# Optimization experiments

Hardware: AMD Instinct MI355X
Metric: run time of the kernel (lower is better)

## Reference

```python
import jax, jax.numpy as jnp
import numpy as np

IN_F = 4096
OUT_F = 4096
NNZ = 1638400
TOKENS = 8192


def setup_inputs() -> dict:
    key = jax.random.key(0)
    k1, k2, k3, k4, k5 = jax.random.split(key, 5)
    x = jax.random.normal(k1, (TOKENS, IN_F), dtype=jnp.float32)
    weight_pruned = jax.random.normal(k2, (NNZ,), dtype=jnp.float32)
    bias = jax.random.normal(k3, (OUT_F,), dtype=jnp.float32)
    row_idx = jax.random.randint(k4, (NNZ,), 0, OUT_F, dtype=jnp.int32)
    col_idx = jax.random.randint(k5, (NNZ,), 0, IN_F, dtype=jnp.int32)
    return {"x": x, "weight_pruned": weight_pruned, "bias": bias,
            "row_idx": row_idx, "col_idx": col_idx}


def reference(x, weight_pruned, bias, row_idx, col_idx):
    # matching torch advanced-index assignment), then dense linear.
    W = jnp.zeros((OUT_F, IN_F), dtype=weight_pruned.dtype)
    W = W.at[row_idx, col_idx].set(weight_pruned)
    return x @ W.T + bias
```

## Files before the change

### kernel.cpp

```cpp
#include <hip/hip_runtime.h>
#include <hip/hip_bf16.h>
#include <cstdint>

#define TOKENS 8192
#define IN_F 4096
#define OUT_F 4096

typedef __bf16 bf16x8 __attribute__((ext_vector_type(8)));
typedef float f32x4 __attribute__((ext_vector_type(4)));

__global__ void scatter_max_kernel(const int* __restrict__ row,
                                   const int* __restrict__ col,
                                   int* __restrict__ M, int nnz) {
    int i = blockIdx.x * blockDim.x + threadIdx.x;
    if (i < nnz) {
        atomicMax(&M[(size_t)row[i] * IN_F + col[i]], i);
    }
}

__global__ void extract_convert_kernel(const int* __restrict__ M,
                                       const float* __restrict__ w,
                                       __bf16* __restrict__ Wb,
                                       const float* __restrict__ x,
                                       __bf16* __restrict__ xb,
                                       int eb) {
    if ((int)blockIdx.x < eb) {
        size_t base = ((size_t)blockIdx.x * 256 + threadIdx.x) * 8;
        int4 m0 = *(const int4*)(M + base);
        int4 m1 = *(const int4*)(M + base + 4);
        int idx[8] = {m0.x, m0.y, m0.z, m0.w, m1.x, m1.y, m1.z, m1.w};
        bf16x8 o;
#pragma unroll
        for (int j = 0; j < 8; ++j) {
            o[j] = (idx[j] >= 0) ? (__bf16)w[idx[j]] : (__bf16)0.0f;
        }
        *(bf16x8*)(Wb + base) = o;
    } else {
        size_t base = ((size_t)(blockIdx.x - eb) * 256 + threadIdx.x) * 8;
        float4 v0 = *(const float4*)(x + base);
        float4 v1 = *(const float4*)(x + base + 4);
        bf16x8 o;
        o[0] = (__bf16)v0.x; o[1] = (__bf16)v0.y;
        o[2] = (__bf16)v0.z; o[3] = (__bf16)v0.w;
        o[4] = (__bf16)v1.x; o[5] = (__bf16)v1.y;
        o[6] = (__bf16)v1.z; o[7] = (__bf16)v1.w;
        *(bf16x8*)(xb + base) = o;
    }
}

__global__ __launch_bounds__(256) void gemm_bt_kernel(
    const __bf16* __restrict__ A,
    const __bf16* __restrict__ B,
    const float* __restrict__ bias,
    float* __restrict__ C) {
    __shared__ __bf16 As[128 * 32];
    __shared__ __bf16 Bs[128 * 32];

    const int tid  = threadIdx.x;
    const int lane = tid & 63;
    const int wid  = tid >> 6;
    const int m0 = blockIdx.y * 128;
    const int n0 = blockIdx.x * 128;
    const int wm = (wid >> 1) * 64;
    const int wn = (wid & 1) * 64;

    const int srow = lane >> 2;
    const int scol = (((lane & 3) ^ ((lane >> 3) & 3)) * 8);
    const int c0 = wid * 2, c1 = wid * 2 + 1;

    const __bf16* ga0 = A + (size_t)(m0 + c0 * 16 + srow) * IN_F + scol;
    const __bf16* ga1 = A + (size_t)(m0 + c1 * 16 + srow) * IN_F + scol;
    const __bf16* gb0 = B + (size_t)(n0 + c0 * 16 + srow) * IN_F + scol;
    const __bf16* gb1 = B + (size_t)(n0 + c1 * 16 + srow) * IN_F + scol;

    __bf16* la0 = &As[c0 * 512];
    __bf16* la1 = &As[c1 * 512];
    __bf16* lb0 = &Bs[c0 * 512];
    __bf16* lb1 = &Bs[c1 * 512];

    const int fm = lane & 15;
    const int fc = (((lane >> 4) ^ ((fm >> 1) & 3)) * 8);
    const __bf16* fa = &As[(wm + fm) * 32 + fc];
    const __bf16* fb = &Bs[(wn + fm) * 32 + fc];

    f32x4 acc[4][4] = {};

    for (int kt = 0; kt < IN_F; kt += 32) {
        __builtin_amdgcn_global_load_lds(
            (unsigned int __attribute__((address_space(1)))*)(ga0 + kt),
            (unsigned int __attribute__((address_space(3)))*)la0, 16, 0, 0);
        __builtin_amdgcn_global_load_lds(
            (unsigned int __attribute__((address_space(1)))*)(ga1 + kt),
            (unsigned int __attribute__((address_space(3)))*)la1, 16, 0, 0);
        __builtin_amdgcn_global_load_lds(
            (unsigned int __attribute__((address_space(1)))*)(gb0 + kt),
            (unsigned int __attribute__((address_space(3)))*)lb0, 16, 0, 0);
        __builtin_amdgcn_global_load_lds(
            (unsigned int __attribute__((address_space(1)))*)(gb1 + kt),
            (unsigned int __attribute__((address_space(3)))*)lb1, 16, 0, 0);

        __syncthreads();

        bf16x8 afrag[4], bfrag[4];
#pragma unroll
        for (int t = 0; t < 4; ++t) afrag[t] = *(const bf16x8*)(fa + t * 512);
#pragma unroll
        for (int t = 0; t < 4; ++t) bfrag[t] = *(const bf16x8*)(fb + t * 512);

#pragma unroll
        for (int mt = 0; mt < 4; ++mt)
#pragma unroll
            for (int nt = 0; nt < 4; ++nt)
                acc[mt][nt] = __builtin_amdgcn_mfma_f32_16x16x32_bf16(
                    afrag[mt], bfrag[nt], acc[mt][nt], 0, 0, 0);

        __syncthreads();
    }

    float bv[4];
#pragma unroll
    for (int nt = 0; nt < 4; ++nt) bv[nt] = bias[n0 + wn + nt * 16 + fm];
    const int r0 = m0 + wm + (lane >> 4) * 4;
#pragma unroll
    for (int mt = 0; mt < 4; ++mt)
#pragma unroll
        for (int nt = 0; nt < 4; ++nt) {
            const int cc = n0 + wn + nt * 16 + fm;
#pragma unroll
            for (int i = 0; i < 4; ++i) {
                C[(size_t)(r0 + mt * 16 + i) * OUT_F + cc] = acc[mt][nt][i] + bv[nt];
            }
        }
}

extern "C" void kernel_launch(void* const* d_in, const int* in_sizes, int n_in,
                              void* d_out, int out_size, void* d_ws, size_t ws_size,
                              hipStream_t stream) {
    const float* x    = (const float*)d_in[0];
    const float* w    = (const float*)d_in[1];
    const float* bias = (const float*)d_in[2];
    const int*   row  = (const int*)d_in[3];
    const int*   col  = (const int*)d_in[4];
    float* out = (float*)d_out;
    const int nnz = in_sizes[3];

    __bf16* xb = (__bf16*)d_ws;
    __bf16* Wb = (__bf16*)((char*)d_ws + (size_t)TOKENS * IN_F * 2);
    int* M = (int*)d_out;

    hipMemsetAsync(M, 0xFF, (size_t)OUT_F * IN_F * 4, stream);

    scatter_max_kernel<<<(nnz + 255) / 256, 256, 0, stream>>>(row, col, M, nnz);

    const int eb = OUT_F * IN_F / (256 * 8);
    const int cb = TOKENS * IN_F / (256 * 8);
    extract_convert_kernel<<<eb + cb, 256, 0, stream>>>(M, w, Wb, x, xb, eb);

    dim3 grid(OUT_F / 128, TOKENS / 128);
    gemm_bt_kernel<<<grid, 256, 0, stream>>>(xb, Wb, bias, out);
}
```

Measured before the change: 625.0 us.

## Replace GEMM with 256x256-tile double-buffered pipelined MFMA kernel

Replaces the 128x128, BK=32, single-buffered bf16 GEMM with a 256x256 tile, BK=64 kernel using 512 threads. It double-buffers the A/B tiles in 128 KB of dynamic LDS, interleaves global-to-LDS loads with MFMA phases, raises wave priority during MFMA, and swizzles block order for L2 locality. The goal is to hide load latency and raise arithmetic intensity in the GEMM, which dominates the runtime. The cost is heavy LDS use that limits occupancy, many barriers, and a hand-tuned schedule that depends on exact waitcnt counts.

```diff
diff --git a/kernel.cpp b/kernel.cpp
--- a/kernel.cpp
+++ b/kernel.cpp
@@ -48,89 +48,134 @@
     }
 }
 
-__global__ __launch_bounds__(256) void gemm_bt_kernel(
+#define BK 64
+#define NT (IN_F / BK)
+
+__global__ __launch_bounds__(512, 2) void gemm256_kernel(
     const __bf16* __restrict__ A,
     const __bf16* __restrict__ B,
     const float* __restrict__ bias,
     float* __restrict__ C) {
-    __shared__ __bf16 As[128 * 32];
-    __shared__ __bf16 Bs[128 * 32];
-
-    const int tid  = threadIdx.x;
-    const int lane = tid & 63;
-    const int wid  = tid >> 6;
-    const int m0 = blockIdx.y * 128;
-    const int n0 = blockIdx.x * 128;
-    const int wm = (wid >> 1) * 64;
-    const int wn = (wid & 1) * 64;
-
-    const int srow = lane >> 2;
-    const int scol = (((lane & 3) ^ ((lane >> 3) & 3)) * 8);
-    const int c0 = wid * 2, c1 = wid * 2 + 1;
-
-    const __bf16* ga0 = A + (size_t)(m0 + c0 * 16 + srow) * IN_F + scol;
-    const __bf16* ga1 = A + (size_t)(m0 + c1 * 16 + srow) * IN_F + scol;
-    const __bf16* gb0 = B + (size_t)(n0 + c0 * 16 + srow) * IN_F + scol;
-    const __bf16* gb1 = B + (size_t)(n0 + c1 * 16 + srow) * IN_F + scol;
-
-    __bf16* la0 = &As[c0 * 512];
-    __bf16* la1 = &As[c1 * 512];
-    __bf16* lb0 = &Bs[c0 * 512];
-    __bf16* lb1 = &Bs[c1 * 512];
-
-    const int fm = lane & 15;
-    const int fc = (((lane >> 4) ^ ((fm >> 1) & 3)) * 8);
-    const __bf16* fa = &As[(wm + fm) * 32 + fc];
-    const __bf16* fb = &Bs[(wn + fm) * 32 + fc];
-
-    f32x4 acc[4][4] = {};
-
-    for (int kt = 0; kt < IN_F; kt += 32) {
-        __builtin_amdgcn_global_load_lds(
-            (unsigned int __attribute__((address_space(1)))*)(ga0 + kt),
-            (unsigned int __attribute__((address_space(3)))*)la0, 16, 0, 0);
-        __builtin_amdgcn_global_load_lds(
-            (unsigned int __attribute__((address_space(1)))*)(ga1 + kt),
-            (unsigned int __attribute__((address_space(3)))*)la1, 16, 0, 0);
-        __builtin_amdgcn_global_load_lds(
-            (unsigned int __attribute__((address_space(1)))*)(gb0 + kt),
-            (unsigned int __attribute__((address_space(3)))*)lb0, 16, 0, 0);
-        __builtin_amdgcn_global_load_lds(
-            (unsigned int __attribute__((address_space(1)))*)(gb1 + kt),
-            (unsigned int __attribute__((address_space(3)))*)lb1, 16, 0, 0);
-
-        __syncthreads();
-
-        bf16x8 afrag[4], bfrag[4];
-#pragma unroll
-        for (int t = 0; t < 4; ++t) afrag[t] = *(const bf16x8*)(fa + t * 512);
-#pragma unroll
-        for (int t = 0; t < 4; ++t) bfrag[t] = *(const bf16x8*)(fb + t * 512);
-
-#pragma unroll
-        for (int mt = 0; mt < 4; ++mt)
-#pragma unroll
-            for (int nt = 0; nt < 4; ++nt)
-                acc[mt][nt] = __builtin_amdgcn_mfma_f32_16x16x32_bf16(
-                    afrag[mt], bfrag[nt], acc[mt][nt], 0, 0, 0);
-
-        __syncthreads();
-    }
+    extern __shared__ __bf16 sm[];
+
+    const int tid = threadIdx.x;
+    const int l   = tid & 63;
+    const int wid = tid >> 6;
+    const int wm  = wid >> 2;
+    const int wn  = wid & 3;
+
+    const int bid = blockIdx.y * 16 + blockIdx.x;
+    const int swz = (bid & 7) * 64 + (bid >> 3);
+    const int n0 = (swz & 15) * 256;
+    const int m0 = (swz >> 4) * 256;
+
+    const int srow   = tid >> 3;
+    const int schunk = (tid & 7) ^ (srow & 7);
+    const __bf16* gA = A + (size_t)(m0 + srow) * IN_F + schunk * 8;
+    const __bf16* gB = B + (size_t)(n0 + srow) * IN_F + schunk * 8;
+    const int ldsw = wid * 512;
+
+#define GLD(SRC, LEL)                                                          \
+    __builtin_amdgcn_global_load_lds(                                          \
+        (unsigned int __attribute__((address_space(1)))*)(SRC),                \
+        (unsigned int __attribute__((address_space(3)))*)(sm + (LEL)), 16, 0, 0);
+
+#define STAGE_A(BUF, KT) {                                                     \
+    GLD(gA + (KT),              (BUF)*16384 + 0     + ldsw)                    \
+    GLD(gA + 64*IN_F  + (KT),   (BUF)*16384 + 4096  + ldsw)                    \
+    GLD(gA + 128*IN_F + (KT),   (BUF)*16384 + 8192  + ldsw)                    \
+    GLD(gA + 192*IN_F + (KT),   (BUF)*16384 + 12288 + ldsw) }
+
+#define STAGE_B(BUF, KT) {                                                     \
+    GLD(gB + (KT),              32768 + (BUF)*16384 + 0     + ldsw)            \
+    GLD(gB + 64*IN_F  + (KT),   32768 + (BUF)*16384 + 4096  + ldsw)            \
+    GLD(gB + 128*IN_F + (KT),   32768 + (BUF)*16384 + 8192  + ldsw)            \
+    GLD(gB + 192*IN_F + (KT),   32768 + (BUF)*16384 + 12288 + ldsw) }
+
+    const int g    = l >> 4;
+    const int fr   = l & 15;
+    const int ch0  = g ^ (l & 7);
+    const int ch1  = ch0 ^ 4;
+    const int arow = (wm * 128 + fr) * 64;
+    const int brow = (wn * 64 + fr) * 64;
+
+    f32x4 acc[8][4] = {};
+    bf16x8 a[4][2], b[2][2];
+
+#define LDA_H(BUF, MH) {                                                                  \
+    _Pragma("unroll") for (int mf = 0; mf < 4; ++mf) {                                    \
+        a[mf][0] = *(const bf16x8*)(sm + (BUF)*16384 + (MH)*4096 + arow + mf*1024 + ch0*8); \
+        a[mf][1] = *(const bf16x8*)(sm + (BUF)*16384 + (MH)*4096 + arow + mf*1024 + ch1*8); } }
+
+#define LDB_P(BUF, NB) {                                                                  \
+    _Pragma("unroll") for (int j = 0; j < 2; ++j) {                                       \
+        b[j][0] = *(const bf16x8*)(sm + 32768 + (BUF)*16384 + brow + ((NB)+j)*1024 + ch0*8); \
+        b[j][1] = *(const bf16x8*)(sm + 32768 + (BUF)*16384 + brow + ((NB)+j)*1024 + ch1*8); } }
+
+#define MMA(MH, NB) {                                                          \
+    __builtin_amdgcn_s_setprio(1);                                             \
+    _Pragma("unroll") for (int mf = 0; mf < 4; ++mf)                           \
+    _Pragma("unroll") for (int j = 0; j < 2; ++j) {                            \
+        acc[(MH)*4+mf][(NB)+j] = __builtin_amdgcn_mfma_f32_16x16x32_bf16(      \
+            a[mf][0], b[j][0], acc[(MH)*4+mf][(NB)+j], 0, 0, 0);               \
+        acc[(MH)*4+mf][(NB)+j] = __builtin_amdgcn_mfma_f32_16x16x32_bf16(      \
+            a[mf][1], b[j][1], acc[(MH)*4+mf][(NB)+j], 0, 0, 0); }             \
+    __builtin_amdgcn_s_setprio(0); }
+
+#define BARRIER() { asm volatile("" ::: "memory");                             \
+                    __builtin_amdgcn_s_barrier();                              \
+                    asm volatile("" ::: "memory"); }
+#define LGKM0()   asm volatile("s_waitcnt lgkmcnt(0)" ::: "memory");
+#define VMC(N)    asm volatile("s_waitcnt vmcnt(" #N ")" ::: "memory");
+
+    STAGE_A(0, 0)
+    STAGE_B(0, 0)
+    STAGE_A(1, BK)
+    VMC(4)
+    BARRIER()
+
+#pragma unroll 1
+    for (int t = 0; t < NT; t += 2) {
+        const int k1 = (t + 1) * BK;
+        const int k2 = ((t + 2) & (NT - 1)) * BK;
+        const int k3 = ((t + 3) & (NT - 1)) * BK;
+
+        LDA_H(0, 0) LDB_P(0, 0) STAGE_B(1, k1)
+        BARRIER() LGKM0() MMA(0, 0) BARRIER()
+        LDB_P(0, 2)
+        BARRIER() LGKM0() MMA(0, 2) BARRIER()
+        LDA_H(0, 1)
+        BARRIER() LGKM0() MMA(1, 2) BARRIER()
+        LDB_P(0, 0) STAGE_A(0, k2)
+        BARRIER() LGKM0() MMA(1, 0) VMC(4) BARRIER()
+
+        LDA_H(1, 0) LDB_P(1, 0) STAGE_B(0, k2)
+        BARRIER() LGKM0() MMA(0, 0) BARRIER()
+        LDB_P(1, 2)
+        BARRIER() LGKM0() MMA(0, 2) BARRIER()
+        LDA_H(1, 1)
+        BARRIER() LGKM0() MMA(1, 2) BARRIER()
+        LDB_P(1, 0) STAGE_A(1, k3)
+        BARRIER() LGKM0() MMA(1, 0) VMC(4) BARRIER()
+    }
+    VMC(0)
 
     float bv[4];
 #pragma unroll
-    for (int nt = 0; nt < 4; ++nt) bv[nt] = bias[n0 + wn + nt * 16 + fm];
-    const int r0 = m0 + wm + (lane >> 4) * 4;
-#pragma unroll
-    for (int mt = 0; mt < 4; ++mt)
-#pragma unroll
-        for (int nt = 0; nt < 4; ++nt) {
-            const int cc = n0 + wn + nt * 16 + fm;
-#pragma unroll
-            for (int i = 0; i < 4; ++i) {
-                C[(size_t)(r0 + mt * 16 + i) * OUT_F + cc] = acc[mt][nt][i] + bv[nt];
+    for (int nf = 0; nf < 4; ++nf) bv[nf] = bias[n0 + wn * 64 + nf * 16 + fr];
+    const int r0 = m0 + wm * 128 + g * 4;
+#pragma unroll
+    for (int mh = 0; mh < 2; ++mh)
+#pragma unroll
+        for (int mf = 0; mf < 4; ++mf)
+#pragma unroll
+            for (int nf = 0; nf < 4; ++nf) {
+                const int col = n0 + wn * 64 + nf * 16 + fr;
+#pragma unroll
+                for (int i = 0; i < 4; ++i)
+                    C[(size_t)(r0 + mh * 64 + mf * 16 + i) * OUT_F + col] =
+                        acc[mh * 4 + mf][nf][i] + bv[nf];
             }
-        }
 }
 
 extern "C" void kernel_launch(void* const* d_in, const int* in_sizes, int n_in,
@@ -148,6 +193,13 @@
     __bf16* Wb = (__bf16*)((char*)d_ws + (size_t)TOKENS * IN_F * 2);
     int* M = (int*)d_out;
 
+    static bool attr_done = false;
+    if (!attr_done) {
+        hipFuncSetAttribute(reinterpret_cast<const void*>(gemm256_kernel),
+                            hipFuncAttributeMaxDynamicSharedMemorySize, 131072);
+        attr_done = true;
+    }
+
     hipMemsetAsync(M, 0xFF, (size_t)OUT_F * IN_F * 4, stream);
 
     scatter_max_kernel<<<(nnz + 255) / 256, 256, 0, stream>>>(row, col, M, nnz);
@@ -156,6 +208,6 @@
     const int cb = TOKENS * IN_F / (256 * 8);
     extract_convert_kernel<<<eb + cb, 256, 0, stream>>>(M, w, Wb, x, xb, eb);
 
-    dim3 grid(OUT_F / 128, TOKENS / 128);
-    gemm_bt_kernel<<<grid, 256, 0, stream>>>(xb, Wb, bias, out);
-}
+    dim3 grid(OUT_F / 256, TOKENS / 256);
+    gemm256_kernel<<<grid, 512, 131072, stream>>>(xb, Wb, bias, out);
+}
```

Result: faster. 567.2 us (-9.3%).
